# Kernel tuning notes

Measured on AMD Instinct MI355X. Metric: run time of the kernel, lower is better.

## Reference

```python
import jax, jax.numpy as jnp
import numpy as np

TOP_K = 2

def setup_inputs() -> dict:
    key = jax.random.key(0)
    k1, k2, k3, k4 = jax.random.split(key, 4)
    T, H, E, I = 2048, 1024, 16, 768
    x = jax.random.normal(k1, (T, H), dtype=jnp.float32)
    gate_w = jax.random.normal(k2, (E, H), dtype=jnp.float32) * 0.02
    w13 = jax.random.normal(k3, (E, 2 * I, H), dtype=jnp.float32) * 0.02
    w2 = jax.random.normal(k4, (E, H, I), dtype=jnp.float32) * 0.02
    return {"x": x, "gate_w": gate_w, "w13": w13, "w2": w2}


def reference(x, gate_w, w13, w2):
    # x: [T, H] tokens; gate_w: [E, H]; w13: [E, 2I, H]; w2: [E, H, I]
    T, H = x.shape
    E = gate_w.shape[0]
    I = w2.shape[-1]

    # --- route: gate matmul + softmax top-k router (renormalize=True) ---
    router_logits = x @ gate_w.T                                  # [T, E]
    probs = jax.nn.softmax(router_logits.astype(jnp.float32), axis=-1)
    topk_w, topk_ids = jax.lax.top_k(probs, TOP_K)                # [T, K]
    topk_w = topk_w / jnp.sum(topk_w, axis=-1, keepdims=True)     # renormalize
    topk_w = topk_w.astype(x.dtype)

    # dense combine weights [T, E]: scatter top-k weights back (dispatch/combine)
    dense_gates = jnp.zeros((T, E), dtype=x.dtype)
    dense_gates = dense_gates.at[jnp.arange(T)[:, None], topk_ids].add(topk_w)

    # --- apply sparse experts: SwiGLU FFN per expert, combined by gates ---
    def expert_step(acc, packed):
        w13_e, w2_e, g_e = packed        # [2I,H], [H,I], [T]
        h = x @ w13_e.T                  # [T, 2I]
        act = jax.nn.silu(h[:, :I]) * h[:, I:]   # gate_proj * up_proj
        return acc + g_e[:, None] * (act @ w2_e.T), None

    acc0 = jnp.zeros_like(x)
    out, _ = jax.lax.scan(expert_step, acc0, (w13, w2, dense_gates.T))
    return out
```

## Files before the change

kernel.cpp:

```cpp
#include <hip/hip_runtime.h>
#include <hip/hip_fp16.h>
#include <math.h>

#define T_TOK 2048
#define HDIM  1024
#define NEXP  16
#define IDIM  768
#define BM    128
#define BK    64
#define MAXROWS 6144

#define NW13  (NEXP * 2 * IDIM * HDIM)
#define NW2   (NEXP * HDIM * IDIM)
#define NWTOT (NW13 + NW2)

using f16   = _Float16;
using f16x8 = __attribute__((ext_vector_type(8))) _Float16;
using f32x4 = __attribute__((ext_vector_type(4))) float;

__device__ __forceinline__ f16x8 cvt2(float4 a, float4 b) {
    f16x8 r;
    r[0] = (f16)a.x; r[1] = (f16)a.y; r[2] = (f16)a.z; r[3] = (f16)a.w;
    r[4] = (f16)b.x; r[5] = (f16)b.y; r[6] = (f16)b.z; r[7] = (f16)b.w;
    return r;
}

__device__ __forceinline__ void gload16(const f16* g, f16* l) {
    __builtin_amdgcn_global_load_lds(
        (const __attribute__((address_space(1))) unsigned int*)g,
        (__attribute__((address_space(3))) unsigned int*)l,
        16, 0, 0);
}

__global__ __launch_bounds__(256) void router_kernel(
    const float* __restrict__ x, const float* __restrict__ gw,
    int* __restrict__ tok_e, float* __restrict__ tok_w, int* __restrict__ cnt)
{
    int wave = threadIdx.x >> 6;
    int lane = threadIdx.x & 63;
    int t = blockIdx.x * 4 + wave;
    if (t >= T_TOK) return;

    const float* xrow = x + (size_t)t * HDIM;
    float xv[16];
#pragma unroll
    for (int j = 0; j < 16; ++j) xv[j] = xrow[lane + 64 * j];

    float logits[NEXP];
#pragma unroll
    for (int e = 0; e < NEXP; ++e) {
        const float* gr = gw + (size_t)e * HDIM;
        float s = 0.f;
#pragma unroll
        for (int j = 0; j < 16; ++j) s += xv[j] * gr[lane + 64 * j];
#pragma unroll
        for (int o = 32; o > 0; o >>= 1) s += __shfl_xor(s, o, 64);
        logits[e] = s;
    }

    int i1 = 0; float m1 = logits[0];
#pragma unroll
    for (int e = 1; e < NEXP; ++e) if (logits[e] > m1) { m1 = logits[e]; i1 = e; }
    int i2 = -1; float m2 = -3.0e38f;
#pragma unroll
    for (int e = 0; e < NEXP; ++e) if (e != i1 && logits[e] > m2) { m2 = logits[e]; i2 = e; }

    float w1 = 1.f / (1.f + expf(m2 - m1));
    float w2 = 1.f - w1;

    if (lane == 0) {
        tok_e[t * 2 + 0] = i1; tok_e[t * 2 + 1] = i2;
        tok_w[t * 2 + 0] = w1; tok_w[t * 2 + 1] = w2;
        atomicAdd(&cnt[i1], 1);
        atomicAdd(&cnt[i2], 1);
    }
}

__global__ void prefix_kernel(const int* __restrict__ cnt, int* __restrict__ base,
                              int* __restrict__ total)
{
    if (threadIdx.x == 0) {
        int b = 0;
        for (int e = 0; e < NEXP; ++e) {
            base[e] = b;
            b += (cnt[e] + BM - 1) & ~(BM - 1);
        }
        base[NEXP] = b;
        *total = b;
    }
}

__global__ __launch_bounds__(256) void scatter_kernel(
    const int* __restrict__ tok_e, const float* __restrict__ tok_w,
    const int* __restrict__ base, int* __restrict__ cnt2,
    int* __restrict__ rowslot, float* __restrict__ rowgate)
{
    int t = blockIdx.x * 256 + threadIdx.x;
    if (t >= T_TOK) return;
#pragma unroll
    for (int k = 0; k < 2; ++k) {
        int e = tok_e[t * 2 + k];
        int pos = atomicAdd(&cnt2[e], 1);
        int row = base[e] + pos;
        rowslot[row] = t * 2 + k;
        rowgate[row] = tok_w[t * 2 + k];
    }
}

__global__ __launch_bounds__(256) void wcast_kernel(
    const float* __restrict__ w13, const float* __restrict__ w2,
    f16* __restrict__ w13h, f16* __restrict__ w2h)
{
    size_t stride = (size_t)gridDim.x * 256 * 8;
    for (size_t i8 = ((size_t)blockIdx.x * 256 + threadIdx.x) * 8; i8 < (size_t)NWTOT; i8 += stride) {
        const float* src; f16* dst; size_t off;
        if (i8 < (size_t)NW13) { src = w13; dst = w13h; off = i8; }
        else                   { src = w2;  dst = w2h;  off = i8 - NW13; }
        float4 a = *(const float4*)(src + off);
        float4 b = *(const float4*)(src + off + 4);
        *(f16x8*)(dst + off) = cvt2(a, b);
    }
}

__global__ __launch_bounds__(256) void xpack_kernel(
    const float* __restrict__ x, const int* __restrict__ rowslot,
    const int* __restrict__ base, const int* __restrict__ cnt,
    f16* __restrict__ xg)
{
    int gid = blockIdx.x * 256 + threadIdx.x;
    int row = gid >> 7, c8 = (gid & 127) * 8;
    int e = 0;
#pragma unroll
    for (int i = 1; i < NEXP; ++i) if (base[i] <= row) e = i;
    f16x8 o = {};
    if ((unsigned)(row - base[e]) < (unsigned)cnt[e]) {
        int tok = rowslot[row] >> 1;
        const float* p = x + (size_t)tok * HDIM + c8;
        o = cvt2(*(const float4*)p, *(const float4*)(p + 4));
    }
    *(f16x8*)&xg[(size_t)row * HDIM + c8] = o;
}

__global__ __launch_bounds__(512, 4) void gemm1_kernel(
    const f16* __restrict__ xg, const f16* __restrict__ w13h,
    const int* __restrict__ base, const int* __restrict__ total,
    f16* __restrict__ act)
{
    int lin = blockIdx.x + blockIdx.y * 12;
    int swz = (lin % 8) * 72 + (lin / 8);
    int chunk = swz / 12;
    int mb = (chunk % 6) * 8 + (chunk / 6);
    int nt = swz % 12;

    int row0 = mb * BM;
    if (row0 >= *total) return;

    int e = 0;
#pragma unroll
    for (int i = 1; i < NEXP; ++i) if (base[i] <= row0) e = i;

    __shared__ f16 a_sm[128 * 64];
    __shared__ f16 b_sm[128 * 64];

    int tid = threadIdx.x;
    int r0 = tid >> 3;
    int cg = (tid & 7) * 8;

    const f16* ga0 = xg + (size_t)(row0 + r0) * HDIM + cg;
    const f16* ga1 = xg + (size_t)(row0 + 64 + r0) * HDIM + cg;
    const f16* wbase = w13h + (size_t)e * 2 * IDIM * HDIM;
    const f16* gb0 = wbase + (size_t)(nt * 64 + r0) * HDIM + cg;
    const f16* gb1 = wbase + (size_t)(IDIM + nt * 64 + r0) * HDIM + cg;

    int wv = tid >> 6, lane = tid & 63, l16 = lane & 15, lk = lane >> 4;
    int wr = wv >> 1;
    int wc = wv & 1;

    f32x4 acc[2][4] = {};

    for (int k0 = 0; k0 < HDIM; k0 += BK) {
        __syncthreads();
        gload16(ga0 + k0, &a_sm[tid * 8]);
        gload16(ga1 + k0, &a_sm[4096 + tid * 8]);
        gload16(gb0 + k0, &b_sm[tid * 8]);
        gload16(gb1 + k0, &b_sm[4096 + tid * 8]);
        __syncthreads();
#pragma unroll
        for (int ks = 0; ks < 2; ++ks) {
            f16x8 af[2], bf[4];
#pragma unroll
            for (int m = 0; m < 2; ++m)
                af[m] = *(const f16x8*)&a_sm[(wr * 32 + m * 16 + l16) * 64 + ks * 32 + lk * 8];
#pragma unroll
            for (int n = 0; n < 2; ++n) {
                bf[n]     = *(const f16x8*)&b_sm[(wc * 32 + n * 16 + l16) * 64 + ks * 32 + lk * 8];
                bf[n + 2] = *(const f16x8*)&b_sm[(64 + wc * 32 + n * 16 + l16) * 64 + ks * 32 + lk * 8];
            }
#pragma unroll
            for (int m = 0; m < 2; ++m)
#pragma unroll
                for (int n = 0; n < 4; ++n)
                    acc[m][n] = __builtin_amdgcn_mfma_f32_16x16x32_f16(af[m], bf[n], acc[m][n], 0, 0, 0);
        }
    }

#pragma unroll
    for (int m = 0; m < 2; ++m)
#pragma unroll
        for (int n = 0; n < 2; ++n)
#pragma unroll
            for (int j = 0; j < 4; ++j) {
                float hg = acc[m][n][j];
                float hu = acc[m][n + 2][j];
                float sg = hg / (1.f + expf(-hg));
                int row = row0 + wr * 32 + m * 16 + lk * 4 + j;
                act[(size_t)row * IDIM + nt * 64 + wc * 32 + n * 16 + l16] = (f16)(sg * hu);
            }
}

__global__ __launch_bounds__(512, 4) void gemm2_kernel(
    const f16* __restrict__ act, const f16* __restrict__ w2h,
    const int* __restrict__ rowslot, const float* __restrict__ rowgate,
    const int* __restrict__ base, const int* __restrict__ cnt, const int* __restrict__ total,
    float* __restrict__ out)
{
    int lin = blockIdx.x + blockIdx.y * 16;
    int swz = (lin % 8) * 96 + (lin / 8);
    int chunk = swz / 16;
    int mb = (chunk % 6) * 8 + (chunk / 6);
    int nt = swz % 16;

    int row0 = mb * BM;
    if (row0 >= *total) return;

    int e = 0;
#pragma unroll
    for (int i = 1; i < NEXP; ++i) if (base[i] <= row0) e = i;
    int basee = base[e], cnte = cnt[e];

    __shared__ f16 a_sm[128 * 64];
    __shared__ f16 b_sm[64 * 64];

    int tid = threadIdx.x;
    int r0 = tid >> 3, cg = (tid & 7) * 8;

    const f16* ga0 = act + (size_t)(row0 + r0) * IDIM + cg;
    const f16* ga1 = act + (size_t)(row0 + 64 + r0) * IDIM + cg;
    const f16* gb0 = w2h + (size_t)e * HDIM * IDIM + (size_t)(nt * 64 + r0) * IDIM + cg;

    int wv = tid >> 6, lane = tid & 63, l16 = lane & 15, lk = lane >> 4;
    int wr = wv >> 1, wc = wv & 1;

    f32x4 acc[2][2] = {};

    for (int k0 = 0; k0 < IDIM; k0 += BK) {
        __syncthreads();
        gload16(ga0 + k0, &a_sm[tid * 8]);
        gload16(ga1 + k0, &a_sm[4096 + tid * 8]);
        gload16(gb0 + k0, &b_sm[tid * 8]);
        __syncthreads();
#pragma unroll
        for (int ks = 0; ks < 2; ++ks) {
            f16x8 af[2], bf[2];
#pragma unroll
            for (int m = 0; m < 2; ++m)
                af[m] = *(const f16x8*)&a_sm[(wr * 32 + m * 16 + l16) * 64 + ks * 32 + lk * 8];
#pragma unroll
            for (int n = 0; n < 2; ++n)
                bf[n] = *(const f16x8*)&b_sm[(wc * 32 + n * 16 + l16) * 64 + ks * 32 + lk * 8];
#pragma unroll
            for (int m = 0; m < 2; ++m)
#pragma unroll
                for (int n = 0; n < 2; ++n)
                    acc[m][n] = __builtin_amdgcn_mfma_f32_16x16x32_f16(af[m], bf[n], acc[m][n], 0, 0, 0);
        }
    }

#pragma unroll
    for (int m = 0; m < 2; ++m)
#pragma unroll
        for (int j = 0; j < 4; ++j) {
            int row = row0 + wr * 32 + m * 16 + lk * 4 + j;
            if ((unsigned)(row - basee) < (unsigned)cnte) {
                int sl = rowslot[row];
                float g = rowgate[row];
                float* orow = out + (size_t)(sl >> 1) * HDIM + nt * 64 + wc * 32;
#pragma unroll
                for (int n = 0; n < 2; ++n)
                    atomicAdd(&orow[n * 16 + l16], g * acc[m][n][j]);
            }
        }
}

extern "C" void kernel_launch(void* const* d_in, const int* in_sizes, int n_in,
                              void* d_out, int out_size, void* d_ws, size_t ws_size,
                              hipStream_t stream) {
    const float* x   = (const float*)d_in[0];
    const float* gw  = (const float*)d_in[1];
    const float* w13 = (const float*)d_in[2];
    const float* w2  = (const float*)d_in[3];
    float* out = (float*)d_out;

    char* ws = (char*)d_ws;
    size_t off = 0;
    f16* w13h      = (f16*)(ws + off);   off += (size_t)NW13 * 2;
    f16* w2h       = (f16*)(ws + off);   off += (size_t)NW2 * 2;
    f16* xg        = (f16*)(ws + off);   off += (size_t)MAXROWS * HDIM * 2;
    f16* act       = (f16*)(ws + off);   off += (size_t)MAXROWS * IDIM * 2;
    int* rowslot   = (int*)(ws + off);   off += (size_t)MAXROWS * 4;
    float* rowgate = (float*)(ws + off); off += (size_t)MAXROWS * 4;
    int* tok_e     = (int*)(ws + off);   off += (size_t)T_TOK * 2 * 4;
    float* tok_w   = (float*)(ws + off); off += (size_t)T_TOK * 2 * 4;
    int* cnt       = (int*)(ws + off);   off += 64;
    int* cnt2      = (int*)(ws + off);   off += 64;
    int* base      = (int*)(ws + off);   off += 128;
    int* total     = (int*)(ws + off);   off += 64;

    hipMemsetAsync(cnt, 0, 128, stream);
    hipMemsetAsync(out, 0, (size_t)T_TOK * HDIM * 4, stream);

    router_kernel<<<T_TOK / 4, 256, 0, stream>>>(x, gw, tok_e, tok_w, cnt);
    prefix_kernel<<<1, 64, 0, stream>>>(cnt, base, total);
    scatter_kernel<<<T_TOK / 256, 256, 0, stream>>>(tok_e, tok_w, base, cnt2, rowslot, rowgate);

    wcast_kernel<<<2048, 256, 0, stream>>>(w13, w2, w13h, w2h);
    xpack_kernel<<<(MAXROWS * 128) / 256, 256, 0, stream>>>(x, rowslot, base, cnt, xg);

    dim3 g1(12, 48);
    gemm1_kernel<<<g1, 512, 0, stream>>>(xg, w13h, base, total, act);

    dim3 g2(16, 48);
    gemm2_kernel<<<g2, 512, 0, stream>>>(act, w2h, rowslot, rowgate, base, cnt, total, out);
}
```

Before: 349.8 us.

## Replace gemm2 atomic scatter with fp16 staging buffer and gather-combine kernel

The second GEMM no longer atomically adds gated results into the output. It writes unweighted per-row results as fp16 into a reused staging buffer. A new combine kernel then gathers each token's two expert rows through a token-to-row map, applies the gate weights and writes the output directly, which also removes the output memset. The weight-cast kernel is restructured so separate block ranges handle w13 and w2, with 16 elements per thread and a fixed 3-iteration unroll. The cost is an extra kernel launch, an extra write and read of the staging buffer, and fp16 rounding of the expert outputs before combining.

```diff
diff --git a/kernel.cpp b/kernel.cpp
--- a/kernel.cpp
+++ b/kernel.cpp
@@ -12,7 +12,8 @@
 
 #define NW13  (NEXP * 2 * IDIM * HDIM)
 #define NW2   (NEXP * HDIM * IDIM)
-#define NWTOT (NW13 + NW2)
+#define WB1   2048
+#define WB2   1024
 
 using f16   = _Float16;
 using f16x8 = __attribute__((ext_vector_type(8))) _Float16;
@@ -93,7 +94,7 @@
 __global__ __launch_bounds__(256) void scatter_kernel(
     const int* __restrict__ tok_e, const float* __restrict__ tok_w,
     const int* __restrict__ base, int* __restrict__ cnt2,
-    int* __restrict__ rowslot, float* __restrict__ rowgate)
+    int* __restrict__ rowslot, int* __restrict__ tok2row)
 {
     int t = blockIdx.x * 256 + threadIdx.x;
     if (t >= T_TOK) return;
@@ -103,7 +104,7 @@
         int pos = atomicAdd(&cnt2[e], 1);
         int row = base[e] + pos;
         rowslot[row] = t * 2 + k;
-        rowgate[row] = tok_w[t * 2 + k];
+        tok2row[t * 2 + k] = row;
     }
 }
 
@@ -111,14 +112,18 @@
     const float* __restrict__ w13, const float* __restrict__ w2,
     f16* __restrict__ w13h, f16* __restrict__ w2h)
 {
-    size_t stride = (size_t)gridDim.x * 256 * 8;
-    for (size_t i8 = ((size_t)blockIdx.x * 256 + threadIdx.x) * 8; i8 < (size_t)NWTOT; i8 += stride) {
-        const float* src; f16* dst; size_t off;
-        if (i8 < (size_t)NW13) { src = w13; dst = w13h; off = i8; }
-        else                   { src = w2;  dst = w2h;  off = i8 - NW13; }
-        float4 a = *(const float4*)(src + off);
-        float4 b = *(const float4*)(src + off + 4);
-        *(f16x8*)(dst + off) = cvt2(a, b);
+    const float* src; f16* dst; size_t stride; int inblk;
+    if (blockIdx.x < WB1) { src = w13; dst = w13h; inblk = blockIdx.x;       stride = (size_t)WB1 * 256 * 16; }
+    else                  { src = w2;  dst = w2h;  inblk = blockIdx.x - WB1; stride = (size_t)WB2 * 256 * 16; }
+    size_t p = ((size_t)inblk * 256 + threadIdx.x) * 16;
+#pragma unroll
+    for (int it = 0; it < 3; ++it, p += stride) {
+        float4 a0 = *(const float4*)(src + p);
+        float4 a1 = *(const float4*)(src + p + 4);
+        float4 a2 = *(const float4*)(src + p + 8);
+        float4 a3 = *(const float4*)(src + p + 12);
+        *(f16x8*)(dst + p)     = cvt2(a0, a1);
+        *(f16x8*)(dst + p + 8) = cvt2(a2, a3);
     }
 }
 
@@ -220,9 +225,8 @@
 
 __global__ __launch_bounds__(512, 4) void gemm2_kernel(
     const f16* __restrict__ act, const f16* __restrict__ w2h,
-    const int* __restrict__ rowslot, const float* __restrict__ rowgate,
-    const int* __restrict__ base, const int* __restrict__ cnt, const int* __restrict__ total,
-    float* __restrict__ out)
+    const int* __restrict__ base, const int* __restrict__ total,
+    f16* __restrict__ z)
 {
     int lin = blockIdx.x + blockIdx.y * 16;
     int swz = (lin % 8) * 96 + (lin / 8);
@@ -236,7 +240,6 @@
     int e = 0;
 #pragma unroll
     for (int i = 1; i < NEXP; ++i) if (base[i] <= row0) e = i;
-    int basee = base[e], cnte = cnt[e];
 
     __shared__ f16 a_sm[128 * 64];
     __shared__ f16 b_sm[64 * 64];
@@ -281,15 +284,26 @@
 #pragma unroll
         for (int j = 0; j < 4; ++j) {
             int row = row0 + wr * 32 + m * 16 + lk * 4 + j;
-            if ((unsigned)(row - basee) < (unsigned)cnte) {
-                int sl = rowslot[row];
-                float g = rowgate[row];
-                float* orow = out + (size_t)(sl >> 1) * HDIM + nt * 64 + wc * 32;
-#pragma unroll
-                for (int n = 0; n < 2; ++n)
-                    atomicAdd(&orow[n * 16 + l16], g * acc[m][n][j]);
-            }
+#pragma unroll
+            for (int n = 0; n < 2; ++n)
+                z[(size_t)row * HDIM + nt * 64 + wc * 32 + n * 16 + l16] = (f16)acc[m][n][j];
         }
+}
+
+__global__ __launch_bounds__(256) void combine_kernel(
+    const f16* __restrict__ z, const int* __restrict__ tok2row,
+    const float* __restrict__ tok_w, float* __restrict__ out)
+{
+    int gid = blockIdx.x * 256 + threadIdx.x;
+    int t = gid >> 7, c8 = (gid & 127) * 8;
+    int r0 = tok2row[2 * t], r1 = tok2row[2 * t + 1];
+    float g0 = tok_w[2 * t], g1 = tok_w[2 * t + 1];
+    f16x8 z0 = *(const f16x8*)&z[(size_t)r0 * HDIM + c8];
+    f16x8 z1 = *(const f16x8*)&z[(size_t)r1 * HDIM + c8];
+    float* o = out + (size_t)t * HDIM + c8;
+#pragma unroll
+    for (int i = 0; i < 8; ++i)
+        o[i] = g0 * (float)z0[i] + g1 * (float)z1[i];
 }
 
 extern "C" void kernel_launch(void* const* d_in, const int* in_sizes, int n_in,
@@ -308,27 +322,29 @@
     f16* xg        = (f16*)(ws + off);   off += (size_t)MAXROWS * HDIM * 2;
     f16* act       = (f16*)(ws + off);   off += (size_t)MAXROWS * IDIM * 2;
     int* rowslot   = (int*)(ws + off);   off += (size_t)MAXROWS * 4;
-    float* rowgate = (float*)(ws + off); off += (size_t)MAXROWS * 4;
+    int* tok2row   = (int*)(ws + off);   off += (size_t)T_TOK * 2 * 4;
     int* tok_e     = (int*)(ws + off);   off += (size_t)T_TOK * 2 * 4;
     float* tok_w   = (float*)(ws + off); off += (size_t)T_TOK * 2 * 4;
     int* cnt       = (int*)(ws + off);   off += 64;
     int* cnt2      = (int*)(ws + off);   off += 64;
     int* base      = (int*)(ws + off);   off += 128;
     int* total     = (int*)(ws + off);   off += 64;
+    f16* zbuf      = xg;
 
     hipMemsetAsync(cnt, 0, 128, stream);
-    hipMemsetAsync(out, 0, (size_t)T_TOK * HDIM * 4, stream);
 
     router_kernel<<<T_TOK / 4, 256, 0, stream>>>(x, gw, tok_e, tok_w, cnt);
     prefix_kernel<<<1, 64, 0, stream>>>(cnt, base, total);
-    scatter_kernel<<<T_TOK / 256, 256, 0, stream>>>(tok_e, tok_w, base, cnt2, rowslot, rowgate);
-
-    wcast_kernel<<<2048, 256, 0, stream>>>(w13, w2, w13h, w2h);
+    scatter_kernel<<<T_TOK / 256, 256, 0, stream>>>(tok_e, tok_w, base, cnt2, rowslot, tok2row);
+
+    wcast_kernel<<<WB1 + WB2, 256, 0, stream>>>(w13, w2, w13h, w2h);
     xpack_kernel<<<(MAXROWS * 128) / 256, 256, 0, stream>>>(x, rowslot, base, cnt, xg);
 
     dim3 g1(12, 48);
     gemm1_kernel<<<g1, 512, 0, stream>>>(xg, w13h, base, total, act);
 
     dim3 g2(16, 48);
-    gemm2_kernel<<<g2, 512, 0, stream>>>(act, w2h, rowslot, rowgate, base, cnt, total, out);
-}
+    gemm2_kernel<<<g2, 512, 0, stream>>>(act, w2h, base, total, zbuf);
+
+    combine_kernel<<<(T_TOK * 128) / 256, 256, 0, stream>>>(zbuf, tok2row, tok_w, out);
+}
```

Measured after the change: 342.8 us. 1.02x faster.
